# Performance work log

Measured on AMD Instinct MI355X. Metric: run time of the kernel, lower is better.

## Reference

```python
import jax, jax.numpy as jnp
import numpy as np

ANCHORS = jnp.array([[1.3221, 1.73145], [3.19275, 4.00944], [5.05587, 8.09892],
                     [9.47112, 4.84053], [11.2364, 10.0071]], dtype=jnp.float32)
NUM_ANCHORS = 5
NUM_CLASSES = 20
MAX_BOXES = 50
NOOBJECT_SCALE = 1.0
OBJECT_SCALE = 5.0
COORD_SCALE = 1.0
CLASS_SCALE = 1.0
SIL_THRESH = 0.6


def iou_cwh(b1, b2):
    # boxes as (cx, cy, w, h); matches repo bbox_ious(x1y1x2y2=False)
    x1, y1, w1, h1 = b1[..., 0], b1[..., 1], b1[..., 2], b1[..., 3]
    x2, y2, w2, h2 = b2[..., 0], b2[..., 1], b2[..., 2], b2[..., 3]
    uw = jnp.maximum(x1 + w1 * 0.5, x2 + w2 * 0.5) - jnp.minimum(x1 - w1 * 0.5, x2 - w2 * 0.5)
    uh = jnp.maximum(y1 + h1 * 0.5, y2 + h2 * 0.5) - jnp.minimum(y1 - h1 * 0.5, y2 - h2 * 0.5)
    cw = w1 + w2 - uw
    ch = h1 + h2 - uh
    inter = jnp.where((cw <= 0) | (ch <= 0), 0.0, cw * ch)
    return inter / (w1 * h1 + w2 * h2 - inter)


def setup_inputs() -> dict:
    key = jax.random.key(0)
    k1, k2, k3, k4 = jax.random.split(key, 4)
    nB = 64
    output = jax.random.normal(k1, (nB, NUM_ANCHORS * (5 + NUM_CLASSES), 38, 38), dtype=jnp.float32)
    # target layout per box: (class, x, y, w, h), all normalized; x>0 marks a valid box
    cls_col = jax.random.randint(k2, (nB, MAX_BOXES, 1), 0, NUM_CLASSES).astype(jnp.float32)
    xy = jax.random.uniform(k3, (nB, MAX_BOXES, 2), minval=0.05, maxval=0.95)
    wh = jax.random.uniform(k4, (nB, MAX_BOXES, 2), minval=0.02, maxval=0.3)
    target = jnp.concatenate([cls_col, xy, wh], axis=-1).reshape(nB, MAX_BOXES * 5)
    return {"output": output, "target": target}


def region_loss(output, target):
    nB = output.shape[0]
    nA, nC = NUM_ANCHORS, NUM_CLASSES
    nH, nW = output.shape[2], output.shape[3]
    out = output.reshape(nB, nA, 5 + nC, nH, nW)
    x = jax.nn.sigmoid(out[:, :, 0])
    y = jax.nn.sigmoid(out[:, :, 1])
    w = out[:, :, 2]
    h = out[:, :, 3]
    conf = jax.nn.sigmoid(out[:, :, 4])
    # [nB,nA,nC,nH,nW] -> [nB*nA*nH*nW, nC] (matches torch transpose/view order)
    cls_logits = jnp.transpose(out[:, :, 5:], (0, 1, 3, 4, 2)).reshape(-1, nC)

    sg = jax.lax.stop_gradient
    aw, ah = ANCHORS[:, 0], ANCHORS[:, 1]
    grid_x = jnp.arange(nW, dtype=jnp.float32)[None, None, None, :]
    grid_y = jnp.arange(nH, dtype=jnp.float32)[None, None, :, None]
    px = sg(x) + grid_x
    py = sg(y) + grid_y
    pw = jnp.exp(sg(w)) * aw[None, :, None, None]
    ph = jnp.exp(sg(h)) * ah[None, :, None, None]
    pred_boxes = jnp.stack([px, py, pw, ph], axis=-1)  # [nB,nA,nH,nW,4]

    # ---- build_targets (vectorized) ----
    tgt = sg(target).reshape(nB, MAX_BOXES, 5)
    gcls = tgt[:, :, 0]
    gx = tgt[:, :, 1] * nW
    gy = tgt[:, :, 2] * nH
    gw = tgt[:, :, 3] * nW
    gh = tgt[:, :, 4] * nH
    # loop breaks at first x==0 -> cumulative validity
    valid = jnp.cumprod((tgt[:, :, 1] != 0).astype(jnp.int32), axis=1).astype(bool)

    # silence conf_mask where any-GT IoU > thresh
    pb_flat = pred_boxes.reshape(nB, nA * nH * nW, 4)
    gt_boxes = jnp.stack([gx, gy, gw, gh], axis=-1)  # [nB,50,4]
    ious = iou_cwh(pb_flat[:, :, None, :], gt_boxes[:, None, :, :])  # [nB,nAnc,50]
    ious = jnp.where(valid[:, None, :], ious, 0.0)
    max_iou = jnp.max(ious, axis=2)
    conf_mask = jnp.where(max_iou > SIL_THRESH, 0.0, NOOBJECT_SCALE).reshape(nB, nA, nH, nW)

    # seen < 12800 defaults
    shp = (nB, nA, nH, nW)
    coord_mask = jnp.ones(shp, jnp.float32)
    tx = jnp.full(shp, 0.5, jnp.float32)
    ty = jnp.full(shp, 0.5, jnp.float32)
    tw = jnp.zeros(shp, jnp.float32)
    th = jnp.zeros(shp, jnp.float32)
    tconf = jnp.zeros(shp, jnp.float32)
    tcls = jnp.zeros(shp, jnp.float32)
    cls_mask = jnp.zeros(shp, jnp.float32)

    # best anchor per GT by (0,0,w,h) IoU; argmax keeps first max like the strict '>' loop
    zA = jnp.zeros_like(aw)
    anchor_boxes = jnp.stack([zA, zA, aw, ah], axis=-1)  # [nA,4]
    zg = jnp.zeros_like(gw)
    gt_wh = jnp.stack([zg, zg, gw, gh], axis=-1)  # [nB,50,4]
    a_iou = iou_cwh(gt_wh[:, :, None, :], anchor_boxes[None, None, :, :])  # [nB,50,nA]
    best_n = jnp.argmax(a_iou, axis=2)  # [nB,50]

    gi = jnp.clip(gx.astype(jnp.int32), 0, nW - 1)
    gj = jnp.clip(gy.astype(jnp.int32), 0, nH - 1)
    aw_b = aw[best_n]
    ah_b = ah[best_n]
    tx_v = gx - gi.astype(jnp.float32)
    ty_v = gy - gj.astype(jnp.float32)
    tw_v = jnp.log(gw / aw_b)
    th_v = jnp.log(gh / ah_b)
    b_ix = jnp.arange(nB)
    pred_at = pred_boxes[b_ix[:, None], best_n, gj, gi]  # [nB,50,4]
    iou_gt = iou_cwh(gt_boxes, pred_at)  # [nB,50]

    def step(carry, t):
        cm, clm, tx_, ty_, tw_, th_, tcf, tcl = carry
        bsel = jnp.where(valid[:, t], b_ix, nB)  # out-of-bounds -> dropped
        n, j, i = best_n[:, t], gj[:, t], gi[:, t]
        st = lambda a, v: a.at[bsel, n, j, i].set(v, mode='drop')
        cm = st(cm, jnp.full((nB,), OBJECT_SCALE, jnp.float32))
        clm = st(clm, jnp.ones((nB,), jnp.float32))
        tx_ = st(tx_, tx_v[:, t])
        ty_ = st(ty_, ty_v[:, t])
        tw_ = st(tw_, tw_v[:, t])
        th_ = st(th_, th_v[:, t])
        tcf = st(tcf, iou_gt[:, t])
        tcl = st(tcl, gcls[:, t])
        return (cm, clm, tx_, ty_, tw_, th_, tcf, tcl), None

    init = (conf_mask, cls_mask, tx, ty, tw, th, tconf, tcls)
    (conf_mask, cls_mask, tx, ty, tw, th, tconf, tcls), _ = jax.lax.scan(
        step, init, jnp.arange(MAX_BOXES))

    # ---- losses ----
    cmf = jnp.sqrt(conf_mask)
    loss_x = COORD_SCALE * jnp.sum((x * coord_mask - tx * coord_mask) ** 2) / 2.0
    loss_y = COORD_SCALE * jnp.sum((y * coord_mask - ty * coord_mask) ** 2) / 2.0
    loss_w = COORD_SCALE * jnp.sum((w * coord_mask - tw * coord_mask) ** 2) / 2.0
    loss_h = COORD_SCALE * jnp.sum((h * coord_mask - th * coord_mask) ** 2) / 2.0
    loss_conf = jnp.sum((conf * cmf - tconf * cmf) ** 2) / 2.0
    logp = jax.nn.log_softmax(cls_logits, axis=-1)
    labels = tcls.reshape(-1).astype(jnp.int32)
    ce = -jnp.take_along_axis(logp, labels[:, None], axis=1)[:, 0]
    loss_cls = CLASS_SCALE * jnp.sum(ce * cls_mask.reshape(-1))
    return loss_x + loss_y + loss_w + loss_h + loss_conf + loss_cls


def reference(output, target):
    return region_loss(output, target)
```

## Files before the change

### kernel.cpp

```cpp
#include <hip/hip_runtime.h>
#include <math.h>

#define NA 5
#define NC 20
#define NH 38
#define NW 38
#define MAX_BOXES 50
#define SPAT (NH * NW)
#define CELLS_PER_B (NA * SPAT)
#define OBJECT_SCALE 5.0f
#define NOOBJECT_SCALE 1.0f

__constant__ float c_aw[NA] = {1.3221f, 3.19275f, 5.05587f, 9.47112f, 11.2364f};
__constant__ float c_ah[NA] = {1.73145f, 4.00944f, 8.09892f, 4.84053f, 10.0071f};

struct WinRec { int cell; float tx, ty, tw, th, iou, gcls; int pad; };

__device__ __forceinline__ float sigmoidf_(float v) { return 1.f / (1.f + expf(-v)); }

__device__ __forceinline__ float iou_cwh8(float x1, float y1, float w1, float h1,
                                          float x2, float y2, float w2, float h2) {
  float uw = fmaxf(x1 + w1 * 0.5f, x2 + w2 * 0.5f) - fminf(x1 - w1 * 0.5f, x2 - w2 * 0.5f);
  float uh = fmaxf(y1 + h1 * 0.5f, y2 + h2 * 0.5f) - fminf(y1 - h1 * 0.5f, y2 - h2 * 0.5f);
  float cw = w1 + w2 - uw;
  float ch = h1 + h2 - uh;
  float inter = (cw <= 0.f || ch <= 0.f) ? 0.f : cw * ch;
  return inter / (w1 * h1 + w2 * h2 - inter);
}

__global__ __launch_bounds__(64) void prep_kernel(
    const float* __restrict__ out, const float* __restrict__ target,
    float* __restrict__ gtpre, WinRec* __restrict__ win) {
  int b = blockIdx.x;
  int t = threadIdx.x;
  float cls = 0.f, x = 0.f, y = 0.f, w = 0.f, h = 0.f;
  if (t < MAX_BOXES) {
    const float* tg = target + (size_t)(b * MAX_BOXES + t) * 5;
    cls = tg[0]; x = tg[1]; y = tg[2]; w = tg[3]; h = tg[4];
  }
  unsigned long long nz = __ballot(t < MAX_BOXES && x != 0.f);
  unsigned long long low = (t < 63) ? ((1ull << (t + 1)) - 1ull) : ~0ull;
  bool valid = (t < MAX_BOXES) && ((nz & low) == low);

  float gx = x * NW, gy = y * NH, gw = w * NW, gh = h * NH;

  int best = 0; float bestiou = -1.f;
#pragma unroll
  for (int a = 0; a < NA; ++a) {
    float aiou = iou_cwh8(0.f, 0.f, gw, gh, 0.f, 0.f, c_aw[a], c_ah[a]);
    if (aiou > bestiou) { bestiou = aiou; best = a; }
  }
  int gi = min(max((int)gx, 0), NW - 1);
  int gj = min(max((int)gy, 0), NH - 1);

  const float* base = out + ((size_t)(b * NA + best) * 25) * SPAT + gj * NW + gi;
  float px = sigmoidf_(base[0]) + (float)gi;
  float py = sigmoidf_(base[SPAT]) + (float)gj;
  float pw = expf(base[2 * SPAT]) * c_aw[best];
  float ph = expf(base[3 * SPAT]) * c_ah[best];
  float iou_gt = iou_cwh8(gx, gy, gw, gh, px, py, pw, ph);

  int cell = best * SPAT + gj * NW + gi;
  unsigned long long vm = __ballot(valid);
  bool winner = valid;
  for (int tp = 0; tp < MAX_BOXES; ++tp) {
    int c2 = __shfl(cell, tp);
    if (tp > t && ((vm >> tp) & 1ull) && c2 == cell) winner = false;
  }

  if (t < MAX_BOXES) {
    float* g = gtpre + (size_t)(b * MAX_BOXES + t) * 8;
    if (valid) {
      g[0] = gx - gw * 0.5f; g[1] = gx + gw * 0.5f;
      g[2] = gy - gh * 0.5f; g[3] = gy + gh * 0.5f;
      g[4] = gw; g[5] = gh; g[6] = 0.375f * (gw * gh); g[7] = 0.f;
    } else {
      g[0] = 1e30f; g[1] = 1e30f; g[2] = 1e30f; g[3] = 1e30f;
      g[4] = 1.f; g[5] = 1.f; g[6] = 0.f; g[7] = 0.f;
    }
    WinRec wr;
    wr.cell = winner ? cell : -1;
    wr.tx = gx - (float)gi;
    wr.ty = gy - (float)gj;
    wr.tw = logf(gw / c_aw[best]);
    wr.th = logf(gh / c_ah[best]);
    wr.iou = iou_gt;
    wr.gcls = cls;
    wr.pad = 0;
    win[b * MAX_BOXES + t] = wr;
  }
}

__global__ __launch_bounds__(256) void main_kernel(
    const float* __restrict__ out, const float* __restrict__ gtpre,
    const WinRec* __restrict__ win, float* __restrict__ partials) {
  int b = blockIdx.y;
  int s0 = blockIdx.x * 256;
  int s = s0 + threadIdx.x;

  __shared__ float4 sb_lo[MAX_BOXES];
  __shared__ float4 sb_hi[MAX_BOXES];
  __shared__ int s_wcnt;
  __shared__ int s_wcell[MAX_BOXES];
  __shared__ float s_wdata[MAX_BOXES][6];
  __shared__ float s_red[4];

  if (threadIdx.x == 0) s_wcnt = 0;
  __syncthreads();
  if (threadIdx.x < MAX_BOXES) {
    const float4* g = (const float4*)(gtpre + (size_t)(b * MAX_BOXES + threadIdx.x) * 8);
    sb_lo[threadIdx.x] = g[0];
    sb_hi[threadIdx.x] = g[1];
    WinRec wr = win[b * MAX_BOXES + threadIdx.x];
    if (wr.cell >= s0 && wr.cell < s0 + 256) {
      int k = atomicAdd(&s_wcnt, 1);
      s_wcell[k] = wr.cell;
      s_wdata[k][0] = wr.tx; s_wdata[k][1] = wr.ty; s_wdata[k][2] = wr.tw;
      s_wdata[k][3] = wr.th; s_wdata[k][4] = wr.iou; s_wdata[k][5] = wr.gcls;
    }
  }
  __syncthreads();

  float acc = 0.f;
  if (s < CELLS_PER_B) {
    int a = s / SPAT;
    int r = s - a * SPAT;
    int i = r % NW;
    int j = r / NW;
    const float* base = out + ((size_t)(b * NA + a) * 25) * SPAT + r;
    float v0 = base[0];
    float v1 = base[SPAT];
    float v2 = base[2 * SPAT];
    float v3 = base[3 * SPAT];
    float v4 = base[4 * SPAT];
    float xs = sigmoidf_(v0), ys = sigmoidf_(v1), confs = sigmoidf_(v4);
    float pw = expf(v2) * c_aw[a], ph = expf(v3) * c_ah[a];
    float px = xs + (float)i, py = ys + (float)j;
    float plx = px - pw * 0.5f, phx = px + pw * 0.5f;
    float ply = py - ph * 0.5f, phy = py + ph * 0.5f;
    float ap375 = 0.375f * (pw * ph);

    bool suppress = false;
#pragma unroll 10
    for (int t = 0; t < MAX_BOXES; ++t) {
      float4 lo = sb_lo[t];
      float4 hi = sb_hi[t];
      float uw = fmaxf(phx, lo.y) - fminf(plx, lo.x);
      float uh = fmaxf(phy, lo.w) - fminf(ply, lo.z);
      float cw = (pw + hi.x) - uw;
      float ch = (ph + hi.y) - uh;
      float inter = cw * ch;
      suppress = suppress | ((cw > 0.f) & (ch > 0.f) & (inter > (hi.z + ap375)));
    }
    float conf_mask = suppress ? 0.f : NOOBJECT_SCALE;
    float tx = 0.5f, ty = 0.5f, tw = 0.f, th = 0.f, tconf = 0.f;
    float clsloss = 0.f;
    int cnt = s_wcnt;
    for (int k = 0; k < cnt; ++k) {
      if (s_wcell[k] == s) {
        conf_mask = OBJECT_SCALE;
        tx = s_wdata[k][0]; ty = s_wdata[k][1];
        tw = s_wdata[k][2]; th = s_wdata[k][3];
        tconf = s_wdata[k][4];
        int label = (int)s_wdata[k][5];
        const float* cb = base + 5 * SPAT;
        float m = -1e30f, lv = 0.f;
        for (int c = 0; c < NC; ++c) {
          float v = cb[c * SPAT];
          if (c == label) lv = v;
          m = fmaxf(m, v);
        }
        float ssum = 0.f;
        for (int c = 0; c < NC; ++c) ssum += expf(cb[c * SPAT] - m);
        clsloss = (m + logf(ssum)) - lv;
      }
    }
    float dx = xs - tx, dy = ys - ty, dw = v2 - tw, dh = v3 - th, dc = confs - tconf;
    acc = 0.5f * (dx * dx + dy * dy + dw * dw + dh * dh + conf_mask * (dc * dc)) + clsloss;
  }

  for (int o = 32; o > 0; o >>= 1) acc += __shfl_down(acc, o, 64);
  int wid = threadIdx.x >> 6, lane = threadIdx.x & 63;
  if (lane == 0) s_red[wid] = acc;
  __syncthreads();
  if (threadIdx.x == 0)
    partials[blockIdx.y * gridDim.x + blockIdx.x] = s_red[0] + s_red[1] + s_red[2] + s_red[3];
}

__global__ __launch_bounds__(256) void reduce_kernel(
    const float* __restrict__ partials, int n, float* __restrict__ outv) {
  float acc = 0.f;
  for (int i = threadIdx.x; i < n; i += 256) acc += partials[i];
  for (int o = 32; o > 0; o >>= 1) acc += __shfl_down(acc, o, 64);
  __shared__ float s_red[4];
  int wid = threadIdx.x >> 6, lane = threadIdx.x & 63;
  if (lane == 0) s_red[wid] = acc;
  __syncthreads();
  if (threadIdx.x == 0) outv[0] = s_red[0] + s_red[1] + s_red[2] + s_red[3];
}

extern "C" void kernel_launch(void* const* d_in, const int* in_sizes, int n_in,
                              void* d_out, int out_size, void* d_ws, size_t ws_size,
                              hipStream_t stream) {
  const float* out = (const float*)d_in[0];
  const float* target = (const float*)d_in[1];
  int nB = in_sizes[0] / (NA * (5 + NC) * SPAT);

  float* gtpre = (float*)d_ws;
  WinRec* win = (WinRec*)((char*)d_ws + (size_t)nB * MAX_BOXES * 8 * sizeof(float));
  float* partials = (float*)((char*)win + (size_t)nB * MAX_BOXES * sizeof(WinRec));

  int gx = (CELLS_PER_B + 255) / 256;
  hipLaunchKernelGGL(prep_kernel, dim3(nB), dim3(64), 0, stream, out, target, gtpre, win);
  hipLaunchKernelGGL(main_kernel, dim3(gx, nB), dim3(256), 0, stream, out, gtpre, win, partials);
  hipLaunchKernelGGL(reduce_kernel, dim3(1), dim3(256), 0, stream, partials, gx * nB, (float*)d_out);
}
```

Measured before the change: 107.8 us.

## Drop reduce kernel via atomicAdd, read GT boxes directly, simplify IoU test

Removes the separate reduction launch: prep_kernel zeroes the output scalar and each main_kernel block atomically adds its partial sum to it. The ground-truth boxes are now read from global memory (uniform across the block, so likely scalar loads) instead of being staged in shared memory, and the overlap test is rewritten with min/max clamping. This saves one kernel launch and some shared-memory traffic, at the cost of non-deterministic float summation order and ~1k atomics on one address.

```diff
diff --git a/kernel.cpp b/kernel.cpp
--- a/kernel.cpp
+++ b/kernel.cpp
@@ -30,9 +30,10 @@
 
 __global__ __launch_bounds__(64) void prep_kernel(
     const float* __restrict__ out, const float* __restrict__ target,
-    float* __restrict__ gtpre, WinRec* __restrict__ win) {
+    float* __restrict__ gtpre, WinRec* __restrict__ win, float* __restrict__ outv) {
   int b = blockIdx.x;
   int t = threadIdx.x;
+  if (b == 0 && t == 63) outv[0] = 0.f;
   float cls = 0.f, x = 0.f, y = 0.f, w = 0.f, h = 0.f;
   if (t < MAX_BOXES) {
     const float* tg = target + (size_t)(b * MAX_BOXES + t) * 5;
@@ -93,13 +94,11 @@
 
 __global__ __launch_bounds__(256) void main_kernel(
     const float* __restrict__ out, const float* __restrict__ gtpre,
-    const WinRec* __restrict__ win, float* __restrict__ partials) {
+    const WinRec* __restrict__ win, float* __restrict__ outv) {
   int b = blockIdx.y;
   int s0 = blockIdx.x * 256;
   int s = s0 + threadIdx.x;
 
-  __shared__ float4 sb_lo[MAX_BOXES];
-  __shared__ float4 sb_hi[MAX_BOXES];
   __shared__ int s_wcnt;
   __shared__ int s_wcell[MAX_BOXES];
   __shared__ float s_wdata[MAX_BOXES][6];
@@ -108,9 +107,6 @@
   if (threadIdx.x == 0) s_wcnt = 0;
   __syncthreads();
   if (threadIdx.x < MAX_BOXES) {
-    const float4* g = (const float4*)(gtpre + (size_t)(b * MAX_BOXES + threadIdx.x) * 8);
-    sb_lo[threadIdx.x] = g[0];
-    sb_hi[threadIdx.x] = g[1];
     WinRec wr = win[b * MAX_BOXES + threadIdx.x];
     if (wr.cell >= s0 && wr.cell < s0 + 256) {
       int k = atomicAdd(&s_wcnt, 1);
@@ -140,17 +136,17 @@
     float ply = py - ph * 0.5f, phy = py + ph * 0.5f;
     float ap375 = 0.375f * (pw * ph);
 
+    const float4* gt4 = (const float4*)(gtpre + (size_t)b * MAX_BOXES * 8);
     bool suppress = false;
 #pragma unroll 10
     for (int t = 0; t < MAX_BOXES; ++t) {
-      float4 lo = sb_lo[t];
-      float4 hi = sb_hi[t];
-      float uw = fmaxf(phx, lo.y) - fminf(plx, lo.x);
-      float uh = fmaxf(phy, lo.w) - fminf(ply, lo.z);
-      float cw = (pw + hi.x) - uw;
-      float ch = (ph + hi.y) - uh;
-      float inter = cw * ch;
-      suppress = suppress | ((cw > 0.f) & (ch > 0.f) & (inter > (hi.z + ap375)));
+      float4 lo = gt4[2 * t];
+      float4 hi = gt4[2 * t + 1];
+      float cw = fminf(phx, lo.y) - fmaxf(plx, lo.x);
+      float ch = fminf(phy, lo.w) - fmaxf(ply, lo.z);
+      cw = fmaxf(cw, 0.f);
+      ch = fmaxf(ch, 0.f);
+      suppress = suppress | (cw * ch > hi.z + ap375);
     }
     float conf_mask = suppress ? 0.f : NOOBJECT_SCALE;
     float tx = 0.5f, ty = 0.5f, tw = 0.f, th = 0.f, tconf = 0.f;
@@ -184,19 +180,7 @@
   if (lane == 0) s_red[wid] = acc;
   __syncthreads();
   if (threadIdx.x == 0)
-    partials[blockIdx.y * gridDim.x + blockIdx.x] = s_red[0] + s_red[1] + s_red[2] + s_red[3];
-}
-
-__global__ __launch_bounds__(256) void reduce_kernel(
-    const float* __restrict__ partials, int n, float* __restrict__ outv) {
-  float acc = 0.f;
-  for (int i = threadIdx.x; i < n; i += 256) acc += partials[i];
-  for (int o = 32; o > 0; o >>= 1) acc += __shfl_down(acc, o, 64);
-  __shared__ float s_red[4];
-  int wid = threadIdx.x >> 6, lane = threadIdx.x & 63;
-  if (lane == 0) s_red[wid] = acc;
-  __syncthreads();
-  if (threadIdx.x == 0) outv[0] = s_red[0] + s_red[1] + s_red[2] + s_red[3];
+    atomicAdd(outv, s_red[0] + s_red[1] + s_red[2] + s_red[3]);
 }
 
 extern "C" void kernel_launch(void* const* d_in, const int* in_sizes, int n_in,
@@ -208,10 +192,8 @@
 
   float* gtpre = (float*)d_ws;
   WinRec* win = (WinRec*)((char*)d_ws + (size_t)nB * MAX_BOXES * 8 * sizeof(float));
-  float* partials = (float*)((char*)win + (size_t)nB * MAX_BOXES * sizeof(WinRec));
 
   int gx = (CELLS_PER_B + 255) / 256;
-  hipLaunchKernelGGL(prep_kernel, dim3(nB), dim3(64), 0, stream, out, target, gtpre, win);
-  hipLaunchKernelGGL(main_kernel, dim3(gx, nB), dim3(256), 0, stream, out, gtpre, win, partials);
-  hipLaunchKernelGGL(reduce_kernel, dim3(1), dim3(256), 0, stream, partials, gx * nB, (float*)d_out);
+  hipLaunchKernelGGL(prep_kernel, dim3(nB), dim3(64), 0, stream, out, target, gtpre, win, (float*)d_out);
+  hipLaunchKernelGGL(main_kernel, dim3(gx, nB), dim3(256), 0, stream, out, gtpre, win, (float*)d_out);
 }
```

After: 118.1 us. +9.6%, slower.
